# Kernel tuning notes

Hardware: AMD Instinct MI355X
Metric: run time of the kernel (lower is better)

The kernel has to match this reference:

```python
import jax, jax.numpy as jnp
import numpy as np

B, S, V, D, E, F, H, HS, TOPK = 8, 512, 32000, 1024, 8, 4096, 8, 128, 2
NEG = -1e9


def _ln(x, g, b):
    m = x.mean(-1, keepdims=True)
    v = jnp.var(x, axis=-1, keepdims=True)
    return (x - m) * jax.lax.rsqrt(v + 1e-5) * g + b


def _attn(x, Wq, Wk, Wv, Wo, bo):
    q = (x @ Wq).reshape(B, S, H, HS)
    k = (x @ Wk).reshape(B, S, H, HS)
    v = (x @ Wv).reshape(B, S, H, HS)
    att = jnp.einsum('bqhd,bkhd->bhqk', q, k) * (HS ** -0.5)
    causal = jnp.tril(jnp.ones((S, S), bool))
    att = jax.nn.softmax(jnp.where(causal, att, NEG), axis=-1)
    o = jnp.einsum('bhqk,bkhd->bqhd', att, v).reshape(B, S, H * HS)
    return o @ Wo + bo


def _moe(x, noise, Wr, br, Wn, bn, W1, b1, W2, b2):
    # NoisyTopkRouter: logits + randn * softplus(noise_logits), top-k, -inf fill, softmax
    logits = x @ Wr + br                                   # [B,S,E]
    noisy = logits + noise * jax.nn.softplus(x @ Wn + bn)
    _, idx = jax.lax.top_k(noisy, TOPK)                    # [B,S,K]
    mask = jax.nn.one_hot(idx, E, dtype=jnp.bool_).any(-2)  # [B,S,E]
    gate = jax.nn.softmax(jnp.where(mask, noisy, NEG), axis=-1)
    # dense all-expert FFN; combine with gate (gate==0 for non-selected experts,
    # so this equals the original sparse per-expert dispatch/scatter math)
    xf = x.reshape(-1, D)                                   # [T,D]
    gf = gate.reshape(-1, E)                                # [T,E]
    h = jax.nn.relu(jnp.einsum('td,edf->etf', xf, W1) + b1[:, None, :])
    y = jnp.einsum('etf,efd->etd', h, W2) + b2[:, None, :]
    out = jnp.einsum('etd,te->td', y, gf).reshape(x.shape)
    return out, gate


def setup_inputs() -> dict:
    key = jax.random.key(0)
    ks = jax.random.split(key, 24)
    n = lambda i, shp, sc=0.02: jax.random.normal(ks[i], shp, jnp.float32) * sc
    return dict(
        input_ids=jax.random.randint(ks[0], (B, S), 0, V),
        attention_mask=jnp.ones((B, S), jnp.int32),
        emb=n(1, (V, D), 1.0),
        pos=n(2, (1, S, D), 1.0),
        Wq=n(3, (D, H * HS)), Wk=n(4, (D, H * HS)), Wv=n(5, (D, H * HS)),
        Wo=n(6, (H * HS, D)), bo=jnp.zeros((D,)),
        g1=jnp.ones((D,)), be1=jnp.zeros((D,)),
        g2=jnp.ones((D,)), be2=jnp.zeros((D,)),
        g3=jnp.ones((D,)), be3=jnp.zeros((D,)),
        Wr1=n(7, (D, E)), br1=jnp.zeros((E,)), Wn1=n(8, (D, E)), bn1=jnp.zeros((E,)),
        W1a=n(9, (E, D, F)), b1a=jnp.zeros((E, F)), W2a=n(10, (E, F, D)), b2a=jnp.zeros((E, D)),
        Wr2=n(11, (D, E)), br2=jnp.zeros((E,)), Wn2=n(12, (D, E)), bn2=jnp.zeros((E,)),
        W1b=n(13, (E, D, F)), b1b=jnp.zeros((E, F)), W2b=n(14, (E, F, D)), b2b=jnp.zeros((E, D)),
        noise1=jax.random.normal(ks[15], (B, S, E), jnp.float32),
        noise2=jax.random.normal(ks[16], (B, S, E), jnp.float32),
        Wc=n(17, (D, 10)), bc=jnp.zeros((10,)),
    )


def reference(input_ids, attention_mask, emb, pos, Wq, Wk, Wv, Wo, bo,
              g1, be1, g2, be2, g3, be3,
              Wr1, br1, Wn1, bn1, W1a, b1a, W2a, b2a,
              Wr2, br2, Wn2, bn2, W1b, b1b, W2b, b2b,
              noise1, noise2, Wc, bc):
    x = emb[input_ids]                                     # [B,S,D]
    x = x + _attn(_ln(x, g1, be1), Wq, Wk, Wv, Wo, bo)
    x = x + pos                                            # dropout = identity (eval)
    first, _ = _moe(_ln(x, g2, be2), noise1, Wr1, br1, Wn1, bn1, W1a, b1a, W2a, b2a)
    second, _ = _moe(_ln(x, g3, be3), noise2, Wr2, br2, Wn2, bn2, W1b, b1b, W2b, b2b)
    feature = second.mean(axis=1)                          # [B,D]
    cls = feature @ Wc + bc                                # [B,10]
    return (first, second, feature, cls)
```

## Files before the change

kernel.cpp:

```cpp
#include <hip/hip_runtime.h>
#include <cstdint>

typedef unsigned short u16;
typedef __attribute__((ext_vector_type(8))) __bf16 bf16x8;
typedef __attribute__((ext_vector_type(4))) float f32x4;

#define TOK 4096
#define DM  1024
#define EXP 8
#define FF  4096
#define SEQ 512
#define NH  8
#define HD  128
#define JOBCAP 9216

__device__ __forceinline__ u16 f2bf(float f) {
  union { float f; unsigned int u; } v; v.f = f;
  unsigned int u = v.u;
  u += 0x7FFFu + ((u >> 16) & 1u);
  return (u16)(u >> 16);
}
__device__ __forceinline__ float bf2f(u16 h) {
  union { unsigned int u; float f; } v; v.u = ((unsigned int)h) << 16; return v.f;
}

__device__ __forceinline__ void gl_lds16(const u16* g, u16* l) {
  __builtin_amdgcn_global_load_lds(
      (const __attribute__((address_space(1))) unsigned int*)g,
      (__attribute__((address_space(3))) unsigned int*)l, 16, 0, 0);
}

__global__ void k_embed(const int* __restrict__ ids, const float* __restrict__ emb,
                        float* __restrict__ x) {
  int t = blockIdx.x;
  int id = ids[t];
  const float4* src = (const float4*)(emb + (size_t)id * DM);
  float4* dst = (float4*)(x + (size_t)t * DM);
  dst[threadIdx.x] = src[threadIdx.x];
}

__global__ void k_ln(const float* __restrict__ in, const float* __restrict__ g,
                     const float* __restrict__ be, u16* __restrict__ obf) {
  int t = blockIdx.x, tid = threadIdx.x;
  float4 v = ((const float4*)(in + (size_t)t * DM))[tid];
  float s = v.x + v.y + v.z + v.w;
  float sq = v.x*v.x + v.y*v.y + v.z*v.z + v.w*v.w;
  for (int o = 32; o; o >>= 1) { s += __shfl_down(s, o); sq += __shfl_down(sq, o); }
  __shared__ float ss[4], sqs[4];
  if ((tid & 63) == 0) { ss[tid >> 6] = s; sqs[tid >> 6] = sq; }
  __syncthreads();
  s  = ss[0] + ss[1] + ss[2] + ss[3];
  sq = sqs[0] + sqs[1] + sqs[2] + sqs[3];
  float mean = s * (1.f / DM);
  float var  = sq * (1.f / DM) - mean * mean;
  float rstd = rsqrtf(var + 1e-5f);
  float4 gg = ((const float4*)g)[tid];
  float4 bb = ((const float4*)be)[tid];
  ushort4 u;
  u.x = f2bf((v.x - mean) * rstd * gg.x + bb.x);
  u.y = f2bf((v.y - mean) * rstd * gg.y + bb.y);
  u.z = f2bf((v.z - mean) * rstd * gg.z + bb.z);
  u.w = f2bf((v.w - mean) * rstd * gg.w + bb.w);
  ((ushort4*)(obf + (size_t)t * DM))[tid] = u;
}

__global__ void k_ln2(const float* __restrict__ in, const float* __restrict__ g,
                      const float* __restrict__ be, u16* __restrict__ oh,
                      u16* __restrict__ ol) {
  int t = blockIdx.x, tid = threadIdx.x;
  float4 v = ((const float4*)(in + (size_t)t * DM))[tid];
  float s = v.x + v.y + v.z + v.w;
  float sq = v.x*v.x + v.y*v.y + v.z*v.z + v.w*v.w;
  for (int o = 32; o; o >>= 1) { s += __shfl_down(s, o); sq += __shfl_down(sq, o); }
  __shared__ float ss[4], sqs[4];
  if ((tid & 63) == 0) { ss[tid >> 6] = s; sqs[tid >> 6] = sq; }
  __syncthreads();
  s  = ss[0] + ss[1] + ss[2] + ss[3];
  sq = sqs[0] + sqs[1] + sqs[2] + sqs[3];
  float mean = s * (1.f / DM);
  float var  = sq * (1.f / DM) - mean * mean;
  float rstd = rsqrtf(var + 1e-5f);
  float4 gg = ((const float4*)g)[tid];
  float4 bb = ((const float4*)be)[tid];
  float o4[4];
  o4[0] = (v.x - mean) * rstd * gg.x + bb.x;
  o4[1] = (v.y - mean) * rstd * gg.y + bb.y;
  o4[2] = (v.z - mean) * rstd * gg.z + bb.z;
  o4[3] = (v.w - mean) * rstd * gg.w + bb.w;
  ushort4 uh, ul;
  u16* ph = (u16*)&uh; u16* pl = (u16*)&ul;
  #pragma unroll
  for (int i = 0; i < 4; i++) {
    u16 hi = f2bf(o4[i]); ph[i] = hi; pl[i] = f2bf(o4[i] - bf2f(hi));
  }
  ((ushort4*)(oh + (size_t)t * DM))[tid] = uh;
  ((ushort4*)(ol + (size_t)t * DM))[tid] = ul;
}

__global__ void k_tcvt_split(const float* __restrict__ src, u16* __restrict__ dh,
                             u16* __restrict__ dl, int K, int N) {
  __shared__ float t[32][33];
  int k0 = blockIdx.x * 32, n0 = blockIdx.y * 32;
  int tx = threadIdx.x, ty = threadIdx.y;
  #pragma unroll
  for (int i = 0; i < 4; i++) t[ty + 8*i][tx] = src[(size_t)(k0 + ty + 8*i) * N + n0 + tx];
  __syncthreads();
  int u = ty * 32 + tx;
  int r = u >> 3, kq = u & 7;
  ushort4 oh, ol;
  u16* ph = (u16*)&oh; u16* pl = (u16*)&ol;
  #pragma unroll
  for (int i = 0; i < 4; i++) {
    float v = t[kq*4+i][r];
    u16 hi = f2bf(v); ph[i] = hi; pl[i] = f2bf(v - bf2f(hi));
  }
  *(ushort4*)&dh[(size_t)(n0 + r) * K + k0 + kq*4] = oh;
  *(ushort4*)&dl[(size_t)(n0 + r) * K + k0 + kq*4] = ol;
}

__global__ void k_tcvt(const float* __restrict__ src, u16* __restrict__ dst, int K, int N) {
  __shared__ float t[32][33];
  size_t zoff = (size_t)blockIdx.z * K * N;
  src += zoff;
  u16* d = dst + zoff;
  int k0 = blockIdx.x * 32, n0 = blockIdx.y * 32;
  int tx = threadIdx.x, ty = threadIdx.y;
  #pragma unroll
  for (int i = 0; i < 4; i++) t[ty + 8*i][tx] = src[(size_t)(k0 + ty + 8*i) * N + n0 + tx];
  __syncthreads();
  int u = ty * 32 + tx;
  int r = u >> 3, kq = u & 7;
  ushort4 o;
  o.x = f2bf(t[kq*4+0][r]); o.y = f2bf(t[kq*4+1][r]);
  o.z = f2bf(t[kq*4+2][r]); o.w = f2bf(t[kq*4+3][r]);
  *(ushort4*)&d[(size_t)(n0 + r) * K + k0 + kq*4] = o;
}

__global__ void k_softmax_h(float* __restrict__ scores) {
  int q = blockIdx.x, bh = blockIdx.y, tid = threadIdx.x;
  float* row = scores + ((size_t)bh * 512 + q) * 512;
  u16* orow = (u16*)row;
  const float scale = 0.088388347648318447f;
  int j0 = tid * 2;
  float v0 = -1e30f, v1 = -1e30f;
  if (j0 <= q)     v0 = row[j0] * scale;
  if (j0 + 1 <= q) v1 = row[j0 + 1] * scale;
  float m = fmaxf(v0, v1);
  for (int o = 32; o; o >>= 1) m = fmaxf(m, __shfl_down(m, o));
  __shared__ float sm[4], ssum[4];
  if ((tid & 63) == 0) sm[tid >> 6] = m;
  __syncthreads();
  m = fmaxf(fmaxf(sm[0], sm[1]), fmaxf(sm[2], sm[3]));
  float p0 = (j0 <= q)     ? expf(v0 - m) : 0.f;
  float p1 = (j0 + 1 <= q) ? expf(v1 - m) : 0.f;
  float s = p0 + p1;
  for (int o = 32; o; o >>= 1) s += __shfl_down(s, o);
  if ((tid & 63) == 0) ssum[tid >> 6] = s;
  __syncthreads();
  s = ssum[0] + ssum[1] + ssum[2] + ssum[3];
  float inv = 1.f / s;
  float pi0 = p0 * inv, pi1 = p1 * inv;
  u16 h0 = f2bf(pi0), h1 = f2bf(pi1);
  orow[j0]       = h0; orow[j0 + 1]       = h1;
  orow[512 + j0] = f2bf(pi0 - bf2f(h0));
  orow[512 + j0 + 1] = f2bf(pi1 - bf2f(h1));
}

constexpr int HOP_QKV    = 0;
constexpr int HOP_SCORES = 1;
constexpr int HOP_PV     = 2;
constexpr int HOP_PROJ   = 3;

struct GemmHArgs {
  const u16 *Ah, *Al, *Bh, *Bl;
  u16 *D0h, *D0l, *D1h, *D1l, *D2h, *D2l;
  float *Cf;
  const float *bias, *resid, *pos;
  int lda, ldb, K;
};

template<int OP>
__launch_bounds__(256)
__global__ void gemm_h(GemmHArgs p) {
  int bx, by, z;
  if constexpr (OP == HOP_QKV) {
    int bid = blockIdx.x; int xcd = bid & 7, slot = bid >> 3;
    by = xcd * 3 + (slot >> 5); bx = slot & 31; z = 0;
  } else if constexpr (OP == HOP_PROJ) {
    int bid = blockIdx.x; by = bid & 7; bx = bid >> 3; z = 0;
  } else if constexpr (OP == HOP_SCORES) {
    int bid = blockIdx.x; z = bid / 10; int t = bid % 10;
    bx = (t >= 6) ? 3 : (t >= 3) ? 2 : (t >= 1) ? 1 : 0;
    by = t - ((bx * (bx + 1)) >> 1);
  } else {
    bx = blockIdx.x; by = blockIdx.y; z = blockIdx.z;
  }

  const u16 *Ahb, *Alb, *Bhb, *Blb;
  if constexpr (OP == HOP_SCORES) {
    size_t off = (size_t)(z >> 3) * 524288 + (size_t)(z & 7) * 128;
    Ahb = p.Ah + off; Alb = p.Al + off; Bhb = p.Bh + off; Blb = p.Bl + off;
  } else if constexpr (OP == HOP_PV) {
    size_t aoff = (size_t)z * 524288;
    Ahb = p.Ah + aoff; Alb = p.Ah + aoff + 512;
    size_t boff = (size_t)z * 65536;
    Bhb = p.Bh + boff; Blb = p.Bl + boff;
  } else {
    Ahb = p.Ah; Alb = p.Al; Bhb = p.Bh; Blb = p.Bl;
  }

  int kmax = p.K;
  if constexpr (OP == HOP_PV) { int lim = bx * 128 + 128; kmax = lim < p.K ? lim : p.K; }
  int nt = kmax >> 5;

  __shared__ __align__(16) u16 As[2 * 4096];
  __shared__ __align__(16) u16 Bs[2 * 4096];

  int tid = threadIdx.x, lane = tid & 63, wid = tid >> 6;
  int srow = wid * 16 + (lane >> 2), skoff = (lane & 3) * 8;
  int lo0 = (wid * 16) * 32, lo1 = ((wid + 4) * 16) * 32;
  int wr = wid >> 1, wc = wid & 1, fm = lane & 15, fk = (lane >> 4) * 8;

  f32x4 acc[4][4] = {};
  const size_t lda = p.lda, ldb = p.ldb;

  #pragma unroll 1
  for (int pass = 0; pass < 3; ++pass) {
    const u16* Ab = (pass < 2) ? Ahb : Alb;
    const u16* Bb = (pass & 1) ? Blb : Bhb;
    const u16* aptr0 = Ab + (size_t)(bx * 128 + srow) * lda + skoff;
    const u16* aptr1 = Ab + (size_t)(bx * 128 + 64 + srow) * lda + skoff;
    const u16* bptr0 = Bb + (size_t)(by * 128 + srow) * ldb + skoff;
    const u16* bptr1 = Bb + (size_t)(by * 128 + 64 + srow) * ldb + skoff;

    gl_lds16(aptr0, &As[lo0]); gl_lds16(aptr1, &As[lo1]);
    gl_lds16(bptr0, &Bs[lo0]); gl_lds16(bptr1, &Bs[lo1]);
    __syncthreads();
    int cur = 0;
    for (int t = 0; t < nt; ++t) {
      if (t + 1 < nt) {
        int nxt = (cur ^ 1) * 4096;
        int k0 = (t + 1) * 32;
        gl_lds16(aptr0 + k0, &As[nxt + lo0]); gl_lds16(aptr1 + k0, &As[nxt + lo1]);
        gl_lds16(bptr0 + k0, &Bs[nxt + lo0]); gl_lds16(bptr1 + k0, &Bs[nxt + lo1]);
      }
      int cb = cur * 4096;
      bf16x8 af[4], bfr[4];
      #pragma unroll
      for (int i = 0; i < 4; ++i) {
        af[i]  = *(const bf16x8*)&As[cb + (wr * 64 + i * 16 + fm) * 32 + fk];
        bfr[i] = *(const bf16x8*)&Bs[cb + (wc * 64 + i * 16 + fm) * 32 + fk];
      }
      #pragma unroll
      for (int mi = 0; mi < 4; ++mi)
        #pragma unroll
        for (int ni = 0; ni < 4; ++ni)
          acc[mi][ni] = __builtin_amdgcn_mfma_f32_16x16x32_bf16(af[mi], bfr[ni], acc[mi][ni], 0, 0, 0);
      __syncthreads();
      cur ^= 1;
    }
  }

  int rb = (lane >> 4) * 4, cl = lane & 15;
  #pragma unroll
  for (int mi = 0; mi < 4; ++mi)
    #pragma unroll
    for (int ni = 0; ni < 4; ++ni)
      #pragma unroll
      for (int j = 0; j < 4; ++j) {
        int m = bx * 128 + wr * 64 + mi * 16 + rb + j;
        int n = by * 128 + wc * 64 + ni * 16 + cl;
        float v = acc[mi][ni][j];
        if constexpr (OP == HOP_QKV) {
          u16 hi = f2bf(v); u16 lo = f2bf(v - bf2f(hi));
          int sel = n >> 10, nn = n & 1023;
          if (sel == 0) {
            p.D0h[(size_t)m * DM + nn] = hi; p.D0l[(size_t)m * DM + nn] = lo;
          } else if (sel == 1) {
            p.D1h[(size_t)m * DM + nn] = hi; p.D1l[(size_t)m * DM + nn] = lo;
          } else {
            size_t idx = (size_t)((m >> 9) * 8 + (nn >> 7)) * 65536 + (size_t)(nn & 127) * 512 + (m & 511);
            p.D2h[idx] = hi; p.D2l[idx] = lo;
          }
        } else if constexpr (OP == HOP_SCORES) {
          p.Cf[(size_t)z * 262144 + (size_t)m * 512 + n] = v;
        } else if constexpr (OP == HOP_PV) {
          u16 hi = f2bf(v); u16 lo = f2bf(v - bf2f(hi));
          size_t idx = (size_t)(z >> 3) * 524288 + (size_t)m * 1024 + (size_t)(z & 7) * 128 + n;
          p.D0h[idx] = hi; p.D0l[idx] = lo;
        } else {
          size_t idx = (size_t)m * 1024 + n;
          p.Cf[idx] = v + p.bias[n] + p.resid[idx] + p.pos[(size_t)(m & 511) * 1024 + n];
        }
      }
}

constexpr int OP_MOE1 = 0;
constexpr int OP_MOE2 = 1;

struct GemmArgs {
  const u16* A; const u16* B; void* C;
  const float* bias;
  const int* joblist; const int* seg;
  int lda, ldb, K;
};

template<int OP>
__launch_bounds__(256)
__global__ void gemm_k(GemmArgs p) {
  int bid = blockIdx.x;
  int xcd = bid & 7, slot = bid >> 3;
  int bx, by;
  if constexpr (OP == OP_MOE1) {
    by = xcd * 4 + (slot & 3);
    bx = slot >> 2;
  } else {
    bx = xcd * 9 + (slot >> 3);
    by = slot & 7;
  }
  int r0g = bx * 128;
  if (r0g >= p.seg[8]) return;
  int z = 0;
  #pragma unroll
  for (int e = 1; e < 8; ++e) z += (r0g >= p.seg[e]) ? 1 : 0;
  const u16* Bbase = p.B + (size_t)z * 4194304;

  __shared__ __align__(16) u16 As[2 * 4096];
  __shared__ __align__(16) u16 Bs[2 * 4096];

  int tid = threadIdx.x;
  int lane = tid & 63, wid = tid >> 6;

  int srow = wid * 16 + (lane >> 2);
  int skoff = (lane & 3) * 8;

  const u16 *aptr0, *aptr1;
  if constexpr (OP == OP_MOE1) {
    int j0 = p.joblist[r0g + srow];
    int j1 = p.joblist[r0g + 64 + srow];
    aptr0 = p.A + (size_t)(j0 < 0 ? 0 : j0) * p.lda + skoff;
    aptr1 = p.A + (size_t)(j1 < 0 ? 0 : j1) * p.lda + skoff;
  } else {
    aptr0 = p.A + (size_t)(r0g + srow) * p.lda + skoff;
    aptr1 = p.A + (size_t)(r0g + 64 + srow) * p.lda + skoff;
  }
  const u16* bptr0 = Bbase + (size_t)(by * 128 + srow) * p.ldb + skoff;
  const u16* bptr1 = Bbase + (size_t)(by * 128 + 64 + srow) * p.ldb + skoff;

  int lo0 = (wid * 16) * 32;
  int lo1 = ((wid + 4) * 16) * 32;

  int wr = wid >> 1, wc = wid & 1;
  int fm = lane & 15;
  int fk = (lane >> 4) * 8;

  f32x4 acc[4][4] = {};
  int nt = p.K >> 5;

  gl_lds16(aptr0, &As[lo0]); gl_lds16(aptr1, &As[lo1]);
  gl_lds16(bptr0, &Bs[lo0]); gl_lds16(bptr1, &Bs[lo1]);
  __syncthreads();

  int cur = 0;
  for (int t = 0; t < nt; ++t) {
    if (t + 1 < nt) {
      int nxt = (cur ^ 1) * 4096;
      int k0 = (t + 1) * 32;
      gl_lds16(aptr0 + k0, &As[nxt + lo0]); gl_lds16(aptr1 + k0, &As[nxt + lo1]);
      gl_lds16(bptr0 + k0, &Bs[nxt + lo0]); gl_lds16(bptr1 + k0, &Bs[nxt + lo1]);
    }
    int cb = cur * 4096;
    bf16x8 af[4], bfr[4];
    #pragma unroll
    for (int i = 0; i < 4; ++i) {
      af[i]  = *(const bf16x8*)&As[cb + (wr * 64 + i * 16 + fm) * 32 + fk];
      bfr[i] = *(const bf16x8*)&Bs[cb + (wc * 64 + i * 16 + fm) * 32 + fk];
    }
    #pragma unroll
    for (int mi = 0; mi < 4; ++mi)
      #pragma unroll
      for (int ni = 0; ni < 4; ++ni)
        acc[mi][ni] = __builtin_amdgcn_mfma_f32_16x16x32_bf16(af[mi], bfr[ni], acc[mi][ni], 0, 0, 0);
    __syncthreads();
    cur ^= 1;
  }

  int rb = (lane >> 4) * 4;
  int cl = lane & 15;
  #pragma unroll
  for (int mi = 0; mi < 4; ++mi)
    #pragma unroll
    for (int ni = 0; ni < 4; ++ni)
      #pragma unroll
      for (int j = 0; j < 4; ++j) {
        int m = r0g + wr * 64 + mi * 16 + rb + j;
        int n = by * 128 + wc * 64 + ni * 16 + cl;
        float v = acc[mi][ni][j];
        if constexpr (OP == OP_MOE1) {
          float t2 = v + p.bias[(size_t)z * FF + n];
          t2 = t2 > 0.f ? t2 : 0.f;
          ((u16*)p.C)[(size_t)m * FF + n] = f2bf(t2);
        } else {
          ((float*)p.C)[(size_t)m * DM + n] = v + p.bias[(size_t)z * DM + n];
        }
      }
}

__global__ void k_router(const float* __restrict__ xin, const float* __restrict__ g,
                         const float* __restrict__ be,
                         const float* __restrict__ Wr, const float* __restrict__ br,
                         const float* __restrict__ Wn, const float* __restrict__ bn,
                         const float* __restrict__ noise,
                         float* __restrict__ gates, int* __restrict__ topidx) {
  int t = blockIdx.x, tid = threadIdx.x;
  float4 v = ((const float4*)(xin + (size_t)t * DM))[tid];
  float s = v.x + v.y + v.z + v.w;
  float sq = v.x*v.x + v.y*v.y + v.z*v.z + v.w*v.w;
  for (int o = 32; o; o >>= 1) { s += __shfl_down(s, o); sq += __shfl_down(sq, o); }
  __shared__ float ss[4], sqs[4];
  if ((tid & 63) == 0) { ss[tid >> 6] = s; sqs[tid >> 6] = sq; }
  __syncthreads();
  s  = ss[0] + ss[1] + ss[2] + ss[3];
  sq = sqs[0] + sqs[1] + sqs[2] + sqs[3];
  float mean = s * (1.f / DM);
  float var  = sq * (1.f / DM) - mean * mean;
  float rstd = rsqrtf(var + 1e-5f);
  float4 gg = ((const float4*)g)[tid];
  float4 bb = ((const float4*)be)[tid];
  float xl[4];
  xl[0] = (v.x - mean) * rstd * gg.x + bb.x;
  xl[1] = (v.y - mean) * rstd * gg.y + bb.y;
  xl[2] = (v.z - mean) * rstd * gg.z + bb.z;
  xl[3] = (v.w - mean) * rstd * gg.w + bb.w;
  float pl[8], pn[8];
  #pragma unroll
  for (int e = 0; e < 8; e++) { pl[e] = 0.f; pn[e] = 0.f; }
  #pragma unroll
  for (int j = 0; j < 4; j++) {
    int d = tid * 4 + j;
    float xv = xl[j];
    const float4* wr = (const float4*)(Wr + (size_t)d * 8);
    const float4* wn = (const float4*)(Wn + (size_t)d * 8);
    float4 a0 = wr[0], a1 = wr[1], c0 = wn[0], c1 = wn[1];
    pl[0] += xv * a0.x; pl[1] += xv * a0.y; pl[2] += xv * a0.z; pl[3] += xv * a0.w;
    pl[4] += xv * a1.x; pl[5] += xv * a1.y; pl[6] += xv * a1.z; pl[7] += xv * a1.w;
    pn[0] += xv * c0.x; pn[1] += xv * c0.y; pn[2] += xv * c0.z; pn[3] += xv * c0.w;
    pn[4] += xv * c1.x; pn[5] += xv * c1.y; pn[6] += xv * c1.z; pn[7] += xv * c1.w;
  }
  for (int o = 32; o; o >>= 1) {
    #pragma unroll
    for (int e = 0; e < 8; e++) { pl[e] += __shfl_down(pl[e], o); pn[e] += __shfl_down(pn[e], o); }
  }
  __shared__ float sl[4][8], sn[4][8];
  if ((tid & 63) == 0) {
    int w = tid >> 6;
    #pragma unroll
    for (int e = 0; e < 8; e++) { sl[w][e] = pl[e]; sn[w][e] = pn[e]; }
  }
  __syncthreads();
  if (tid == 0) {
    float noisy[8];
    #pragma unroll
    for (int e = 0; e < 8; e++) {
      float l  = sl[0][e] + sl[1][e] + sl[2][e] + sl[3][e] + br[e];
      float nn = sn[0][e] + sn[1][e] + sn[2][e] + sn[3][e] + bn[e];
      float sp = (nn > 20.f) ? nn : log1pf(expf(nn));
      noisy[e] = l + noise[(size_t)t * 8 + e] * sp;
    }
    int i0 = 0;
    for (int e = 1; e < 8; e++) if (noisy[e] > noisy[i0]) i0 = e;
    int i1 = (i0 == 0) ? 1 : 0;
    for (int e = 0; e < 8; e++) if (e != i0 && noisy[e] > noisy[i1]) i1 = e;
    float e1 = expf(noisy[i1] - noisy[i0]);
    float zz = 1.f + e1;
    gates[t * 2] = 1.f / zz; gates[t * 2 + 1] = e1 / zz;
    topidx[t * 2] = i0; topidx[t * 2 + 1] = i1;
  }
}

__global__ void k_moe_init(int* cnt, int* cnt2, int* joblist) {
  int i = blockIdx.x * 256 + threadIdx.x;
  if (i < JOBCAP) joblist[i] = -1;
  if (i < 8) { cnt[i] = 0; cnt2[i] = 0; }
}
__global__ void k_moe_count(const int* __restrict__ topidx, int* __restrict__ cnt) {
  int t = blockIdx.x * 256 + threadIdx.x;
  if (t >= TOK) return;
  atomicAdd(&cnt[topidx[t * 2]], 1);
  atomicAdd(&cnt[topidx[t * 2 + 1]], 1);
}
__global__ void k_moe_offsets(const int* __restrict__ cnt, int* __restrict__ seg) {
  if (threadIdx.x == 0) {
    int o = 0;
    for (int e = 0; e < 8; e++) { seg[e] = o; o += (cnt[e] + 127) & ~127; }
    seg[8] = o;
  }
}
__global__ void k_moe_scatter(const int* __restrict__ topidx, int* __restrict__ cnt2,
                              const int* __restrict__ seg, int* __restrict__ joblist,
                              int* __restrict__ tokpos) {
  int t = blockIdx.x * 256 + threadIdx.x;
  if (t >= TOK) return;
  #pragma unroll
  for (int s = 0; s < 2; s++) {
    int e = topidx[t * 2 + s];
    int p = atomicAdd(&cnt2[e], 1);
    int pos = seg[e] + p;
    joblist[pos] = t;
    tokpos[t * 2 + s] = pos;
  }
}
__global__ void k_combine(const float* __restrict__ y, const float* __restrict__ gates,
                          const int* __restrict__ tokpos, float* __restrict__ out) {
  int t = blockIdx.x, tid = threadIdx.x;
  int p0 = tokpos[t * 2], p1 = tokpos[t * 2 + 1];
  float g0 = gates[t * 2], g1 = gates[t * 2 + 1];
  float4 a = ((const float4*)(y + (size_t)p0 * DM))[tid];
  float4 b = ((const float4*)(y + (size_t)p1 * DM))[tid];
  float4 o;
  o.x = g0 * a.x + g1 * b.x; o.y = g0 * a.y + g1 * b.y;
  o.z = g0 * a.z + g1 * b.z; o.w = g0 * a.w + g1 * b.w;
  ((float4*)(out + (size_t)t * DM))[tid] = o;
}

__global__ void k_feat1(const float* __restrict__ second, float* __restrict__ part) {
  int b = blockIdx.x, c = blockIdx.y, tid = threadIdx.x;
  const float* p = second + ((size_t)b * SEQ + (size_t)c * 64) * DM;
  float4 s = {0.f, 0.f, 0.f, 0.f};
  for (int j = 0; j < 64; ++j) {
    float4 v = ((const float4*)(p + (size_t)j * DM))[tid];
    s.x += v.x; s.y += v.y; s.z += v.z; s.w += v.w;
  }
  ((float4*)(part + (size_t)(b * 8 + c) * DM))[tid] = s;
}
__global__ void k_feat2(const float* __restrict__ part, float* __restrict__ feat) {
  int i = blockIdx.x * 256 + threadIdx.x;
  int b = i >> 10, d = i & 1023;
  float s = 0.f;
  #pragma unroll
  for (int c = 0; c < 8; ++c) s += part[(size_t)(b * 8 + c) * DM + d];
  feat[i] = s * (1.f / SEQ);
}
__global__ void k_cls(const float* __restrict__ feat, const float* __restrict__ Wc,
                      const float* __restrict__ bc, float* __restrict__ cls) {
  int o = blockIdx.x; int b = o / 10, n = o % 10; int l = threadIdx.x;
  float s = 0.f;
  for (int d = l; d < DM; d += 64) s += feat[b * DM + d] * Wc[(size_t)d * 10 + n];
  for (int off = 32; off; off >>= 1) s += __shfl_down(s, off);
  if (l == 0) cls[o] = s + bc[n];
}

extern "C" void kernel_launch(void* const* d_in, const int* in_sizes, int n_in,
                              void* d_out, int out_size, void* d_ws, size_t ws_size,
                              hipStream_t stream) {
  const int*   ids    = (const int*)d_in[0];
  const float* emb    = (const float*)d_in[2];
  const float* pos    = (const float*)d_in[3];
  const float* Wq     = (const float*)d_in[4];
  const float* Wk     = (const float*)d_in[5];
  const float* Wv     = (const float*)d_in[6];
  const float* Wo     = (const float*)d_in[7];
  const float* bo     = (const float*)d_in[8];
  const float* g1     = (const float*)d_in[9];
  const float* be1    = (const float*)d_in[10];
  const float* g2     = (const float*)d_in[11];
  const float* be2    = (const float*)d_in[12];
  const float* g3     = (const float*)d_in[13];
  const float* be3    = (const float*)d_in[14];
  const float* Wr1    = (const float*)d_in[15];
  const float* br1    = (const float*)d_in[16];
  const float* Wn1    = (const float*)d_in[17];
  const float* bn1    = (const float*)d_in[18];
  const float* W1a    = (const float*)d_in[19];
  const float* b1a    = (const float*)d_in[20];
  const float* W2a    = (const float*)d_in[21];
  const float* b2a    = (const float*)d_in[22];
  const float* Wr2    = (const float*)d_in[23];
  const float* br2    = (const float*)d_in[24];
  const float* Wn2    = (const float*)d_in[25];
  const float* bn2    = (const float*)d_in[26];
  const float* W1b    = (const float*)d_in[27];
  const float* b1b    = (const float*)d_in[28];
  const float* W2b    = (const float*)d_in[29];
  const float* b2b    = (const float*)d_in[30];
  const float* noise1 = (const float*)d_in[31];
  const float* noise2 = (const float*)d_in[32];
  const float* Wc     = (const float*)d_in[33];
  const float* bc     = (const float*)d_in[34];

  char* wsp = (char*)d_ws; size_t off = 0;
  auto alloc = [&](size_t bytes) -> void* {
    void* p = wsp + off; off += (bytes + 255) & ~(size_t)255; return p;
  };
  char*  G     = (char*)alloc(180355072);
  float* x     = (float*)alloc((size_t)TOK * DM * 4);
  float* x2    = (float*)alloc((size_t)TOK * DM * 4);
  u16*   xlnb  = (u16*)alloc((size_t)TOK * DM * 2);
  float* gates  = (float*)alloc(TOK * 2 * 4);
  int*   topidx = (int*)alloc(TOK * 2 * 4);
  int*   cnt    = (int*)alloc(8 * 4);
  int*   cnt2   = (int*)alloc(8 * 4);
  int*   seg    = (int*)alloc(16 * 4);
  int*   joblist= (int*)alloc(JOBCAP * 4);
  int*   tokpos = (int*)alloc(TOK * 2 * 4);
  float* fpart  = (float*)alloc(64 * DM * 4);
  (void)ws_size; (void)in_sizes; (void)n_in; (void)out_size;

  u16* WQKVTh = (u16*)(G + 0);
  u16* WQKVTl = (u16*)(G + 6291456);
  u16* WOTh   = (u16*)(G + 12582912);
  u16* WOTl   = (u16*)(G + 14680064);
  u16* XLNH   = (u16*)(G + 16777216);
  u16* XLNL   = (u16*)(G + 25165824);
  u16* QH     = (u16*)(G + 33554432);
  u16* QL     = (u16*)(G + 41943040);
  u16* KH     = (u16*)(G + 50331648);
  u16* KL     = (u16*)(G + 58720256);
  u16* VTh    = (u16*)(G + 67108864);
  u16* VTl    = (u16*)(G + 75497472);
  u16* OH     = (u16*)(G + 83886080);
  u16* OL     = (u16*)(G + 92274688);
  float* SC   = (float*)(G + 100663296);
  u16*   H    = (u16*)(G + 0);
  float* Y    = (float*)(G + 75497472);
  u16*   WBUF = (u16*)(G + 113246208);

  float* out_first  = (float*)d_out;
  float* out_second = out_first + (size_t)TOK * DM;
  float* feat       = out_first + (size_t)2 * TOK * DM;
  float* cls        = feat + 8 * DM;

  dim3 tb(32, 8);
  hipLaunchKernelGGL(k_tcvt_split, dim3(32, 32), tb, 0, stream, Wq, WQKVTh,            WQKVTl,            DM, DM);
  hipLaunchKernelGGL(k_tcvt_split, dim3(32, 32), tb, 0, stream, Wk, WQKVTh + 1048576,  WQKVTl + 1048576,  DM, DM);
  hipLaunchKernelGGL(k_tcvt_split, dim3(32, 32), tb, 0, stream, Wv, WQKVTh + 2097152,  WQKVTl + 2097152,  DM, DM);
  hipLaunchKernelGGL(k_tcvt_split, dim3(32, 32), tb, 0, stream, Wo, WOTh,              WOTl,              DM, DM);
  hipLaunchKernelGGL(k_embed, dim3(TOK), dim3(256), 0, stream, ids, emb, x);
  hipLaunchKernelGGL(k_ln2, dim3(TOK), dim3(256), 0, stream, x, g1, be1, XLNH, XLNL);

  GemmHArgs qa{};
  qa.Ah = XLNH; qa.Al = XLNL; qa.Bh = WQKVTh; qa.Bl = WQKVTl;
  qa.D0h = QH; qa.D0l = QL; qa.D1h = KH; qa.D1l = KL; qa.D2h = VTh; qa.D2l = VTl;
  qa.lda = DM; qa.ldb = DM; qa.K = DM;
  hipLaunchKernelGGL(gemm_h<HOP_QKV>, dim3(768), dim3(256), 0, stream, qa);

  GemmHArgs sa{};
  sa.Ah = QH; sa.Al = QL; sa.Bh = KH; sa.Bl = KL; sa.Cf = SC;
  sa.lda = DM; sa.ldb = DM; sa.K = HD;
  hipLaunchKernelGGL(gemm_h<HOP_SCORES>, dim3(640), dim3(256), 0, stream, sa);
  hipLaunchKernelGGL(k_softmax_h, dim3(SEQ, 64), dim3(256), 0, stream, SC);

  GemmHArgs pa{};
  pa.Ah = (const u16*)SC; pa.Bh = VTh; pa.Bl = VTl;
  pa.D0h = OH; pa.D0l = OL;
  pa.lda = 1024; pa.ldb = 512; pa.K = SEQ;
  hipLaunchKernelGGL(gemm_h<HOP_PV>, dim3(4, 1, 64), dim3(256), 0, stream, pa);

  GemmHArgs pj{};
  pj.Ah = OH; pj.Al = OL; pj.Bh = WOTh; pj.Bl = WOTl; pj.Cf = x2;
  pj.bias = bo; pj.resid = x; pj.pos = pos;
  pj.lda = DM; pj.ldb = DM; pj.K = DM;
  hipLaunchKernelGGL(gemm_h<HOP_PROJ>, dim3(256), dim3(256), 0, stream, pj);

  auto run_moe = [&](const float* g, const float* be, const float* Wr, const float* br,
                     const float* Wn, const float* bn, const float* noise,
                     const float* W1, const float* b1, const float* W2, const float* b2,
                     float* outp) {
    hipLaunchKernelGGL(k_ln, dim3(TOK), dim3(256), 0, stream, x2, g, be, xlnb);
    hipLaunchKernelGGL(k_router, dim3(TOK), dim3(256), 0, stream, x2, g, be, Wr, br, Wn, bn, noise, gates, topidx);
    hipLaunchKernelGGL(k_moe_init, dim3(36), dim3(256), 0, stream, cnt, cnt2, joblist);
    hipLaunchKernelGGL(k_moe_count, dim3(16), dim3(256), 0, stream, topidx, cnt);
    hipLaunchKernelGGL(k_moe_offsets, dim3(1), dim3(64), 0, stream, cnt, seg);
    hipLaunchKernelGGL(k_moe_scatter, dim3(16), dim3(256), 0, stream, topidx, cnt2, seg, joblist, tokpos);
    hipLaunchKernelGGL(k_tcvt, dim3(32, 128, 8), tb, 0, stream, W1, WBUF, DM, FF);
    GemmArgs m1{};
    m1.A = xlnb; m1.B = WBUF; m1.C = H; m1.bias = b1; m1.joblist = joblist; m1.seg = seg;
    m1.lda = DM; m1.ldb = DM; m1.K = DM;
    hipLaunchKernelGGL(gemm_k<OP_MOE1>, dim3(2304), dim3(256), 0, stream, m1);
    hipLaunchKernelGGL(k_tcvt, dim3(128, 32, 8), tb, 0, stream, W2, WBUF, FF, DM);
    GemmArgs m2{};
    m2.A = H; m2.B = WBUF; m2.C = Y; m2.bias = b2; m2.seg = seg;
    m2.lda = FF; m2.ldb = FF; m2.K = FF;
    hipLaunchKernelGGL(gemm_k<OP_MOE2>, dim3(576), dim3(256), 0, stream, m2);
    hipLaunchKernelGGL(k_combine, dim3(TOK), dim3(256), 0, stream, Y, gates, tokpos, outp);
  };
  run_moe(g2, be2, Wr1, br1, Wn1, bn1, noise1, W1a, b1a, W2a, b2a, out_first);
  run_moe(g3, be3, Wr2, br2, Wn2, bn2, noise2, W1b, b1b, W2b, b2b, out_second);

  hipLaunchKernelGGL(k_feat1, dim3(8, 8), dim3(256), 0, stream, out_second, fpart);
  hipLaunchKernelGGL(k_feat2, dim3(32), dim3(256), 0, stream, fpart, feat);
  hipLaunchKernelGGL(k_cls, dim3(80), dim3(64), 0, stream, feat, Wc, bc, cls);
}
```

Before: 1.228 ms.

## Add 256x256-tile pipelined MoE up-projection GEMM with swizzled LDS staging

Replaces the 128x128 templated first expert GEMM with a dedicated 512-thread kernel. It uses 256x256 output tiles, an XOR-swizzled LDS layout in 128 KB of dynamic shared memory, and a four-phase schedule that overlaps global-to-LDS loads with MFMA work, using barriers and priority hints. The goal is more data reuse per loaded tile and better latency hiding in the dominant MoE FFN. Expert segments are now padded to 256 rows, and the job list and workspace grow to match. This pads more rows with wasted work, and the large LDS footprint limits occupancy to one block per CU. The second GEMM is split into its own kernel with a flattened grid mapping.

Result: slower. 1.253 ms (+2.1%).

```diff
diff --git a/kernel.cpp b/kernel.cpp
--- a/kernel.cpp
+++ b/kernel.cpp
@@ -12,7 +12,7 @@
 #define SEQ 512
 #define NH  8
 #define HD  128
-#define JOBCAP 9216
+#define JOBCAP 10496
 
 __device__ __forceinline__ u16 f2bf(float f) {
   union { float f; unsigned int u; } v; v.f = f;
@@ -295,29 +295,142 @@
       }
 }
 
-constexpr int OP_MOE1 = 0;
-constexpr int OP_MOE2 = 1;
+struct GemmM1Args {
+  const u16* A; const u16* B; u16* C;
+  const float* bias;
+  const int* joblist; const int* seg;
+};
+
+__launch_bounds__(512, 2)
+__global__ void gemm_m1(GemmM1Args p) {
+  int bid = blockIdx.x;
+  int xcd = bid & 7, slot = bid >> 3;
+  int by = xcd * 2 + (slot & 1);
+  int bx = slot >> 1;
+  int r0g = bx * 256;
+  if (r0g >= p.seg[8]) return;
+  int z = 0;
+  #pragma unroll
+  for (int e = 1; e < 8; ++e) z += (r0g >= p.seg[e]) ? 1 : 0;
+  const u16* Bb = p.B + (size_t)z * 4194304;
+
+  extern __shared__ u16 sh[];
+
+  int tid = threadIdx.x, lane = tid & 63, wid = tid >> 6;
+  int wr = wid >> 2, wcc = wid & 3;
+
+  int srow = wid * 8 + (lane >> 3);
+  int kk = ((lane & 7) * 8) ^ ((srow & 7) << 3);
+  const u16 *aSrc[2][2], *bSrc[2][2];
+  #pragma unroll
+  for (int h = 0; h < 2; ++h) {
+    int j0 = p.joblist[r0g + h * 128 + srow];
+    int j1 = p.joblist[r0g + h * 128 + 64 + srow];
+    aSrc[h][0] = p.A + (size_t)(j0 < 0 ? 0 : j0) * 1024 + kk;
+    aSrc[h][1] = p.A + (size_t)(j1 < 0 ? 0 : j1) * 1024 + kk;
+    bSrc[h][0] = Bb + (size_t)(by * 256 + h * 128 + srow) * 1024 + kk;
+    bSrc[h][1] = Bb + (size_t)(by * 256 + h * 128 + 64 + srow) * 1024 + kk;
+  }
+  u16* shW = sh + wid * 512;
+
+#define STG_A(T, H) { u16* d_ = shW + ((T)&1)*32768 + (H)*8192;            \
+    gl_lds16(aSrc[H][0] + (T)*64, d_); gl_lds16(aSrc[H][1] + (T)*64, d_ + 4096); }
+#define STG_B(T, H) { u16* d_ = shW + ((T)&1)*32768 + 16384 + (H)*8192;    \
+    gl_lds16(bSrc[H][0] + (T)*64, d_); gl_lds16(bSrc[H][1] + (T)*64, d_ + 4096); }
+#define MM_CLOSE() { __builtin_amdgcn_sched_barrier(0);                    \
+    __builtin_amdgcn_s_barrier(); __builtin_amdgcn_sched_barrier(0); }
+
+  int fm = lane & 15;
+  int swz = (fm & 7) << 3;
+  int kkr0 = ((lane >> 4) * 8) ^ swz;
+  int kkr1 = (32 + (lane >> 4) * 8) ^ swz;
+  int rAbase = (wr * 64 + fm) * 64;
+  int rBbase = (wcc * 32 + fm) * 64;
+
+  f32x4 acc[2][2][4][2] = {};
+
+  STG_A(0,0); STG_B(0,1); STG_A(0,1); STG_B(0,0); STG_A(1,0); STG_B(1,1);
+  asm volatile("s_waitcnt vmcnt(4)" ::: "memory");
+  MM_CLOSE();
+
+#define MM_PHASE(MH, NH, STAGE_CODE) {                                     \
+    int d32 = (t & 1) * 32768;                                             \
+    bf16x8 a_[4][2], b_[2][2];                                             \
+    _Pragma("unroll") for (int mi = 0; mi < 4; ++mi) {                     \
+      a_[mi][0] = *(const bf16x8*)&sh[d32 + (MH)*8192 + rAbase + mi*1024 + kkr0]; \
+      a_[mi][1] = *(const bf16x8*)&sh[d32 + (MH)*8192 + rAbase + mi*1024 + kkr1]; \
+    }                                                                      \
+    _Pragma("unroll") for (int ni = 0; ni < 2; ++ni) {                     \
+      b_[ni][0] = *(const bf16x8*)&sh[d32 + 16384 + (NH)*8192 + rBbase + ni*1024 + kkr0]; \
+      b_[ni][1] = *(const bf16x8*)&sh[d32 + 16384 + (NH)*8192 + rBbase + ni*1024 + kkr1]; \
+    }                                                                      \
+    STAGE_CODE;                                                            \
+    __builtin_amdgcn_sched_barrier(0);                                     \
+    __builtin_amdgcn_s_barrier();                                          \
+    asm volatile("s_waitcnt lgkmcnt(0)" ::: "memory");                     \
+    __builtin_amdgcn_sched_barrier(0);                                     \
+    __builtin_amdgcn_s_setprio(1);                                         \
+    _Pragma("unroll") for (int ks = 0; ks < 2; ++ks)                       \
+      _Pragma("unroll") for (int mi = 0; mi < 4; ++mi)                     \
+        _Pragma("unroll") for (int ni = 0; ni < 2; ++ni)                   \
+          acc[MH][NH][mi][ni] = __builtin_amdgcn_mfma_f32_16x16x32_bf16(   \
+              a_[mi][ks], b_[ni][ks], acc[MH][NH][mi][ni], 0, 0, 0);       \
+    __builtin_amdgcn_s_setprio(0);                                         \
+  }
+
+  #pragma unroll 1
+  for (int t = 0; t < 16; ++t) {
+    int s1 = (t + 1 < 16), s2 = (t + 2 < 16);
+    MM_PHASE(0, 0, { if (s1) STG_A(t + 1, 1); });
+    MM_CLOSE();
+    MM_PHASE(0, 1, { if (s1) STG_B(t + 1, 0); });
+    MM_CLOSE();
+    MM_PHASE(1, 1, { if (s2) STG_A(t + 2, 0); });
+    MM_CLOSE();
+    MM_PHASE(1, 0, { if (s2) STG_B(t + 2, 1); });
+    if (s1) {
+      if (s2) { asm volatile("s_waitcnt vmcnt(4)" ::: "memory"); }
+      else    { asm volatile("s_waitcnt vmcnt(0)" ::: "memory"); }
+    }
+    MM_CLOSE();
+  }
+#undef MM_PHASE
+#undef STG_A
+#undef STG_B
+#undef MM_CLOSE
+
+  int rb = (lane >> 4) * 4, cl = lane & 15;
+  #pragma unroll
+  for (int mh = 0; mh < 2; ++mh)
+    #pragma unroll
+    for (int nh = 0; nh < 2; ++nh)
+      #pragma unroll
+      for (int mi = 0; mi < 4; ++mi)
+        #pragma unroll
+        for (int ni = 0; ni < 2; ++ni)
+          #pragma unroll
+          for (int j = 0; j < 4; ++j) {
+            int m = r0g + mh * 128 + wr * 64 + mi * 16 + rb + j;
+            int n = by * 256 + nh * 128 + wcc * 32 + ni * 16 + cl;
+            float v = acc[mh][nh][mi][ni][j] + p.bias[(size_t)z * FF + n];
+            v = v > 0.f ? v : 0.f;
+            p.C[(size_t)m * FF + n] = f2bf(v);
+          }
+}
 
 struct GemmArgs {
   const u16* A; const u16* B; void* C;
   const float* bias;
-  const int* joblist; const int* seg;
+  const int* seg;
   int lda, ldb, K;
 };
 
-template<int OP>
 __launch_bounds__(256)
-__global__ void gemm_k(GemmArgs p) {
+__global__ void gemm_k2(GemmArgs p) {
   int bid = blockIdx.x;
   int xcd = bid & 7, slot = bid >> 3;
-  int bx, by;
-  if constexpr (OP == OP_MOE1) {
-    by = xcd * 4 + (slot & 3);
-    bx = slot >> 2;
-  } else {
-    bx = xcd * 9 + (slot >> 3);
-    by = slot & 7;
-  }
+  int g = xcd * 82 + slot;
+  int bx = g >> 3, by = g & 7;
   int r0g = bx * 128;
   if (r0g >= p.seg[8]) return;
   int z = 0;
@@ -334,16 +447,8 @@
   int srow = wid * 16 + (lane >> 2);
   int skoff = (lane & 3) * 8;
 
-  const u16 *aptr0, *aptr1;
-  if constexpr (OP == OP_MOE1) {
-    int j0 = p.joblist[r0g + srow];
-    int j1 = p.joblist[r0g + 64 + srow];
-    aptr0 = p.A + (size_t)(j0 < 0 ? 0 : j0) * p.lda + skoff;
-    aptr1 = p.A + (size_t)(j1 < 0 ? 0 : j1) * p.lda + skoff;
-  } else {
-    aptr0 = p.A + (size_t)(r0g + srow) * p.lda + skoff;
-    aptr1 = p.A + (size_t)(r0g + 64 + srow) * p.lda + skoff;
-  }
+  const u16* aptr0 = p.A + (size_t)(r0g + srow) * p.lda + skoff;
+  const u16* aptr1 = p.A + (size_t)(r0g + 64 + srow) * p.lda + skoff;
   const u16* bptr0 = Bbase + (size_t)(by * 128 + srow) * p.ldb + skoff;
   const u16* bptr1 = Bbase + (size_t)(by * 128 + 64 + srow) * p.ldb + skoff;
 
@@ -395,14 +500,7 @@
       for (int j = 0; j < 4; ++j) {
         int m = r0g + wr * 64 + mi * 16 + rb + j;
         int n = by * 128 + wc * 64 + ni * 16 + cl;
-        float v = acc[mi][ni][j];
-        if constexpr (OP == OP_MOE1) {
-          float t2 = v + p.bias[(size_t)z * FF + n];
-          t2 = t2 > 0.f ? t2 : 0.f;
-          ((u16*)p.C)[(size_t)m * FF + n] = f2bf(t2);
-        } else {
-          ((float*)p.C)[(size_t)m * DM + n] = v + p.bias[(size_t)z * DM + n];
-        }
+        ((float*)p.C)[(size_t)m * DM + n] = acc[mi][ni][j] + p.bias[(size_t)z * DM + n];
       }
 }
 
@@ -492,7 +590,7 @@
 __global__ void k_moe_offsets(const int* __restrict__ cnt, int* __restrict__ seg) {
   if (threadIdx.x == 0) {
     int o = 0;
-    for (int e = 0; e < 8; e++) { seg[e] = o; o += (cnt[e] + 127) & ~127; }
+    for (int e = 0; e < 8; e++) { seg[e] = o; o += (cnt[e] + 255) & ~255; }
     seg[8] = o;
   }
 }
@@ -592,7 +690,7 @@
   auto alloc = [&](size_t bytes) -> void* {
     void* p = wsp + off; off += (bytes + 255) & ~(size_t)255; return p;
   };
-  char*  G     = (char*)alloc(180355072);
+  char*  G     = (char*)alloc(196083712);
   float* x     = (float*)alloc((size_t)TOK * DM * 4);
   float* x2    = (float*)alloc((size_t)TOK * DM * 4);
   u16*   xlnb  = (u16*)alloc((size_t)TOK * DM * 2);
@@ -622,8 +720,8 @@
   u16* OL     = (u16*)(G + 92274688);
   float* SC   = (float*)(G + 100663296);
   u16*   H    = (u16*)(G + 0);
-  float* Y    = (float*)(G + 75497472);
-  u16*   WBUF = (u16*)(G + 113246208);
+  float* Y    = (float*)(G + 85983232);
+  u16*   WBUF = (u16*)(G + 128974848);
 
   float* out_first  = (float*)d_out;
   float* out_second = out_first + (size_t)TOK * DM;
@@ -668,20 +766,19 @@
                      float* outp) {
     hipLaunchKernelGGL(k_ln, dim3(TOK), dim3(256), 0, stream, x2, g, be, xlnb);
     hipLaunchKernelGGL(k_router, dim3(TOK), dim3(256), 0, stream, x2, g, be, Wr, br, Wn, bn, noise, gates, topidx);
-    hipLaunchKernelGGL(k_moe_init, dim3(36), dim3(256), 0, stream, cnt, cnt2, joblist);
+    hipLaunchKernelGGL(k_moe_init, dim3(41), dim3(256), 0, stream, cnt, cnt2, joblist);
     hipLaunchKernelGGL(k_moe_count, dim3(16), dim3(256), 0, stream, topidx, cnt);
     hipLaunchKernelGGL(k_moe_offsets, dim3(1), dim3(64), 0, stream, cnt, seg);
     hipLaunchKernelGGL(k_moe_scatter, dim3(16), dim3(256), 0, stream, topidx, cnt2, seg, joblist, tokpos);
     hipLaunchKernelGGL(k_tcvt, dim3(32, 128, 8), tb, 0, stream, W1, WBUF, DM, FF);
-    GemmArgs m1{};
+    GemmM1Args m1{};
     m1.A = xlnb; m1.B = WBUF; m1.C = H; m1.bias = b1; m1.joblist = joblist; m1.seg = seg;
-    m1.lda = DM; m1.ldb = DM; m1.K = DM;
-    hipLaunchKernelGGL(gemm_k<OP_MOE1>, dim3(2304), dim3(256), 0, stream, m1);
+    hipLaunchKernelGGL(gemm_m1, dim3(656), dim3(512), 131072, stream, m1);
     hipLaunchKernelGGL(k_tcvt, dim3(128, 32, 8), tb, 0, stream, W2, WBUF, FF, DM);
     GemmArgs m2{};
     m2.A = H; m2.B = WBUF; m2.C = Y; m2.bias = b2; m2.seg = seg;
     m2.lda = FF; m2.ldb = FF; m2.K = FF;
-    hipLaunchKernelGGL(gemm_k<OP_MOE2>, dim3(576), dim3(256), 0, stream, m2);
+    hipLaunchKernelGGL(gemm_k2, dim3(656), dim3(256), 0, stream, m2);
     hipLaunchKernelGGL(k_combine, dim3(TOK), dim3(256), 0, stream, Y, gates, tokpos, outp);
   };
   run_moe(g2, be2, Wr1, br1, Wn1, bn1, noise1, W1a, b1a, W2a, b2a, out_first);
```

## Batch both MoE layers into single grouped GEMMs over sixteen experts

Applied to the files above, without the earlier changes.

Runs routing, dispatch and both expert GEMMs for the two MoE layers together, treating them as one grouped problem with 16 expert segments instead of two sequential passes of 8. Each grouped GEMM launch gets twice as many tiles, which should reduce partial-wave tail effects and launch and sync overhead between the layers. In exchange the workspace roughly doubles (activations, hidden buffer and weight staging for all 16 experts), and the kernel picks the bias pointer per segment.

Measured after the change: 1.222 ms. No clear change (-0.5%).

```diff
diff --git a/kernel.cpp b/kernel.cpp
--- a/kernel.cpp
+++ b/kernel.cpp
@@ -12,7 +12,7 @@
 #define SEQ 512
 #define NH  8
 #define HD  128
-#define JOBCAP 9216
+#define JOBCAP 18432
 
 __device__ __forceinline__ u16 f2bf(float f) {
   union { float f; unsigned int u; } v; v.f = f;
@@ -300,7 +300,7 @@
 
 struct GemmArgs {
   const u16* A; const u16* B; void* C;
-  const float* bias;
+  const float* b1a; const float* b1b;
   const int* joblist; const int* seg;
   int lda, ldb, K;
 };
@@ -315,15 +315,17 @@
     by = xcd * 4 + (slot & 3);
     bx = slot >> 2;
   } else {
-    bx = xcd * 9 + (slot >> 3);
+    bx = xcd * 18 + (slot >> 3);
     by = slot & 7;
   }
   int r0g = bx * 128;
-  if (r0g >= p.seg[8]) return;
+  if (r0g >= p.seg[16]) return;
   int z = 0;
   #pragma unroll
-  for (int e = 1; e < 8; ++e) z += (r0g >= p.seg[e]) ? 1 : 0;
+  for (int e = 1; e < 16; ++e) z += (r0g >= p.seg[e]) ? 1 : 0;
   const u16* Bbase = p.B + (size_t)z * 4194304;
+  const float* bias = (z < 8) ? p.b1a + (size_t)z * (OP == OP_MOE1 ? FF : DM)
+                              : p.b1b + (size_t)(z - 8) * (OP == OP_MOE1 ? FF : DM);
 
   __shared__ __align__(16) u16 As[2 * 4096];
   __shared__ __align__(16) u16 Bs[2 * 4096];
@@ -397,11 +399,11 @@
         int n = by * 128 + wc * 64 + ni * 16 + cl;
         float v = acc[mi][ni][j];
         if constexpr (OP == OP_MOE1) {
-          float t2 = v + p.bias[(size_t)z * FF + n];
+          float t2 = v + bias[n];
           t2 = t2 > 0.f ? t2 : 0.f;
           ((u16*)p.C)[(size_t)m * FF + n] = f2bf(t2);
         } else {
-          ((float*)p.C)[(size_t)m * DM + n] = v + p.bias[(size_t)z * DM + n];
+          ((float*)p.C)[(size_t)m * DM + n] = v + bias[n];
         }
       }
 }
@@ -481,29 +483,31 @@
 __global__ void k_moe_init(int* cnt, int* cnt2, int* joblist) {
   int i = blockIdx.x * 256 + threadIdx.x;
   if (i < JOBCAP) joblist[i] = -1;
-  if (i < 8) { cnt[i] = 0; cnt2[i] = 0; }
+  if (i < 16) { cnt[i] = 0; cnt2[i] = 0; }
 }
 __global__ void k_moe_count(const int* __restrict__ topidx, int* __restrict__ cnt) {
   int t = blockIdx.x * 256 + threadIdx.x;
-  if (t >= TOK) return;
-  atomicAdd(&cnt[topidx[t * 2]], 1);
-  atomicAdd(&cnt[topidx[t * 2 + 1]], 1);
+  if (t >= 2 * TOK) return;
+  int lo = (t >= TOK) ? 8 : 0;
+  atomicAdd(&cnt[topidx[t * 2] + lo], 1);
+  atomicAdd(&cnt[topidx[t * 2 + 1] + lo], 1);
 }
 __global__ void k_moe_offsets(const int* __restrict__ cnt, int* __restrict__ seg) {
   if (threadIdx.x == 0) {
     int o = 0;
-    for (int e = 0; e < 8; e++) { seg[e] = o; o += (cnt[e] + 127) & ~127; }
-    seg[8] = o;
+    for (int e = 0; e < 16; e++) { seg[e] = o; o += (cnt[e] + 127) & ~127; }
+    seg[16] = o;
   }
 }
 __global__ void k_moe_scatter(const int* __restrict__ topidx, int* __restrict__ cnt2,
                               const int* __restrict__ seg, int* __restrict__ joblist,
                               int* __restrict__ tokpos) {
   int t = blockIdx.x * 256 + threadIdx.x;
-  if (t >= TOK) return;
+  if (t >= 2 * TOK) return;
+  int lo = (t >= TOK) ? 8 : 0;
   #pragma unroll
   for (int s = 0; s < 2; s++) {
-    int e = topidx[t * 2 + s];
+    int e = topidx[t * 2 + s] + lo;
     int p = atomicAdd(&cnt2[e], 1);
     int pos = seg[e] + p;
     joblist[pos] = t;
@@ -592,17 +596,17 @@
   auto alloc = [&](size_t bytes) -> void* {
     void* p = wsp + off; off += (bytes + 255) & ~(size_t)255; return p;
   };
-  char*  G     = (char*)alloc(180355072);
+  char*  G     = (char*)alloc(360710144);
   float* x     = (float*)alloc((size_t)TOK * DM * 4);
   float* x2    = (float*)alloc((size_t)TOK * DM * 4);
-  u16*   xlnb  = (u16*)alloc((size_t)TOK * DM * 2);
-  float* gates  = (float*)alloc(TOK * 2 * 4);
-  int*   topidx = (int*)alloc(TOK * 2 * 4);
-  int*   cnt    = (int*)alloc(8 * 4);
-  int*   cnt2   = (int*)alloc(8 * 4);
-  int*   seg    = (int*)alloc(16 * 4);
+  u16*   xlnb  = (u16*)alloc((size_t)2 * TOK * DM * 2);
+  float* gates  = (float*)alloc(2 * TOK * 2 * 4);
+  int*   topidx = (int*)alloc(2 * TOK * 2 * 4);
+  int*   cnt    = (int*)alloc(16 * 4);
+  int*   cnt2   = (int*)alloc(16 * 4);
+  int*   seg    = (int*)alloc(24 * 4);
   int*   joblist= (int*)alloc(JOBCAP * 4);
-  int*   tokpos = (int*)alloc(TOK * 2 * 4);
+  int*   tokpos = (int*)alloc(2 * TOK * 2 * 4);
   float* fpart  = (float*)alloc(64 * DM * 4);
   (void)ws_size; (void)in_sizes; (void)n_in; (void)out_size;
 
@@ -622,8 +626,8 @@
   u16* OL     = (u16*)(G + 92274688);
   float* SC   = (float*)(G + 100663296);
   u16*   H    = (u16*)(G + 0);
-  float* Y    = (float*)(G + 75497472);
-  u16*   WBUF = (u16*)(G + 113246208);
+  float* Y    = (float*)(G + 150994944);
+  u16*   WBUF = (u16*)(G + 226492416);
 
   float* out_first  = (float*)d_out;
   float* out_second = out_first + (size_t)TOK * DM;
@@ -662,30 +666,35 @@
   pj.lda = DM; pj.ldb = DM; pj.K = DM;
   hipLaunchKernelGGL(gemm_h<HOP_PROJ>, dim3(256), dim3(256), 0, stream, pj);
 
-  auto run_moe = [&](const float* g, const float* be, const float* Wr, const float* br,
-                     const float* Wn, const float* bn, const float* noise,
-                     const float* W1, const float* b1, const float* W2, const float* b2,
-                     float* outp) {
-    hipLaunchKernelGGL(k_ln, dim3(TOK), dim3(256), 0, stream, x2, g, be, xlnb);
-    hipLaunchKernelGGL(k_router, dim3(TOK), dim3(256), 0, stream, x2, g, be, Wr, br, Wn, bn, noise, gates, topidx);
-    hipLaunchKernelGGL(k_moe_init, dim3(36), dim3(256), 0, stream, cnt, cnt2, joblist);
-    hipLaunchKernelGGL(k_moe_count, dim3(16), dim3(256), 0, stream, topidx, cnt);
-    hipLaunchKernelGGL(k_moe_offsets, dim3(1), dim3(64), 0, stream, cnt, seg);
-    hipLaunchKernelGGL(k_moe_scatter, dim3(16), dim3(256), 0, stream, topidx, cnt2, seg, joblist, tokpos);
-    hipLaunchKernelGGL(k_tcvt, dim3(32, 128, 8), tb, 0, stream, W1, WBUF, DM, FF);
-    GemmArgs m1{};
-    m1.A = xlnb; m1.B = WBUF; m1.C = H; m1.bias = b1; m1.joblist = joblist; m1.seg = seg;
-    m1.lda = DM; m1.ldb = DM; m1.K = DM;
-    hipLaunchKernelGGL(gemm_k<OP_MOE1>, dim3(2304), dim3(256), 0, stream, m1);
-    hipLaunchKernelGGL(k_tcvt, dim3(128, 32, 8), tb, 0, stream, W2, WBUF, FF, DM);
-    GemmArgs m2{};
-    m2.A = H; m2.B = WBUF; m2.C = Y; m2.bias = b2; m2.seg = seg;
-    m2.lda = FF; m2.ldb = FF; m2.K = FF;
-    hipLaunchKernelGGL(gemm_k<OP_MOE2>, dim3(576), dim3(256), 0, stream, m2);
-    hipLaunchKernelGGL(k_combine, dim3(TOK), dim3(256), 0, stream, Y, gates, tokpos, outp);
-  };
-  run_moe(g2, be2, Wr1, br1, Wn1, bn1, noise1, W1a, b1a, W2a, b2a, out_first);
-  run_moe(g3, be3, Wr2, br2, Wn2, bn2, noise2, W1b, b1b, W2b, b2b, out_second);
+  hipLaunchKernelGGL(k_ln, dim3(TOK), dim3(256), 0, stream, x2, g2, be2, xlnb);
+  hipLaunchKernelGGL(k_ln, dim3(TOK), dim3(256), 0, stream, x2, g3, be3, xlnb + (size_t)TOK * DM);
+  hipLaunchKernelGGL(k_router, dim3(TOK), dim3(256), 0, stream, x2, g2, be2, Wr1, br1, Wn1, bn1, noise1, gates, topidx);
+  hipLaunchKernelGGL(k_router, dim3(TOK), dim3(256), 0, stream, x2, g3, be3, Wr2, br2, Wn2, bn2, noise2,
+                     gates + (size_t)TOK * 2, topidx + (size_t)TOK * 2);
+  hipLaunchKernelGGL(k_moe_init, dim3(72), dim3(256), 0, stream, cnt, cnt2, joblist);
+  hipLaunchKernelGGL(k_moe_count, dim3(32), dim3(256), 0, stream, topidx, cnt);
+  hipLaunchKernelGGL(k_moe_offsets, dim3(1), dim3(64), 0, stream, cnt, seg);
+  hipLaunchKernelGGL(k_moe_scatter, dim3(32), dim3(256), 0, stream, topidx, cnt2, seg, joblist, tokpos);
+
+  hipLaunchKernelGGL(k_tcvt, dim3(32, 128, 8), tb, 0, stream, W1a, WBUF, DM, FF);
+  hipLaunchKernelGGL(k_tcvt, dim3(32, 128, 8), tb, 0, stream, W1b, WBUF + (size_t)8 * DM * FF, DM, FF);
+  GemmArgs m1{};
+  m1.A = xlnb; m1.B = WBUF; m1.C = H; m1.b1a = b1a; m1.b1b = b1b;
+  m1.joblist = joblist; m1.seg = seg;
+  m1.lda = DM; m1.ldb = DM; m1.K = DM;
+  hipLaunchKernelGGL(gemm_k<OP_MOE1>, dim3(4608), dim3(256), 0, stream, m1);
+
+  hipLaunchKernelGGL(k_tcvt, dim3(128, 32, 8), tb, 0, stream, W2a, WBUF, FF, DM);
+  hipLaunchKernelGGL(k_tcvt, dim3(128, 32, 8), tb, 0, stream, W2b, WBUF + (size_t)8 * DM * FF, FF, DM);
+  GemmArgs m2{};
+  m2.A = H; m2.B = WBUF; m2.C = Y; m2.b1a = b2a; m2.b1b = b2b;
+  m2.joblist = joblist; m2.seg = seg;
+  m2.lda = FF; m2.ldb = FF; m2.K = FF;
+  hipLaunchKernelGGL(gemm_k<OP_MOE2>, dim3(1152), dim3(256), 0, stream, m2);
+
+  hipLaunchKernelGGL(k_combine, dim3(TOK), dim3(256), 0, stream, Y, gates, tokpos, out_first);
+  hipLaunchKernelGGL(k_combine, dim3(TOK), dim3(256), 0, stream, Y,
+                     gates + (size_t)TOK * 2, tokpos + (size_t)TOK * 2, out_second);
 
   hipLaunchKernelGGL(k_feat1, dim3(8, 8), dim3(256), 0, stream, out_second, fpart);
   hipLaunchKernelGGL(k_feat2, dim3(32), dim3(256), 0, stream, fpart, feat);
```
